# Kernel optimization log

Measured on AMD Instinct MI355X. Metric: run time of the kernel, lower is better.

Reference implementation:

```python
import jax, jax.numpy as jnp
import numpy as np

B, S, D, H, DFF, L = 8192, 9, 3, 3, 2048, 3
HD = D // H  # head dim = 1
EPS = 1e-5


def _ln(x, g, b):
    m = jnp.mean(x, axis=-1, keepdims=True)
    v = jnp.var(x, axis=-1, keepdims=True)
    return (x - m) * jax.lax.rsqrt(v + EPS) * g + b


def _encoder_layer(h, Wqkv, bqkv, Wo, bo, g1, b1, W1, bf1, W2, bf2, g2, b2):
    # h: [B,S,D]; post-norm TransformerEncoderLayer (PyTorch defaults, eval mode)
    qkv = jnp.einsum('bsd,ed->bse', h, Wqkv) + bqkv      # [B,S,3D]
    q, k, v = jnp.split(qkv, 3, axis=-1)
    Bv = h.shape[0]
    q = q.reshape(Bv, S, H, HD) * (1.0 / np.sqrt(HD))
    k = k.reshape(Bv, S, H, HD)
    v = v.reshape(Bv, S, H, HD)
    attn = jax.nn.softmax(jnp.einsum('bqhd,bkhd->bhqk', q, k), axis=-1)
    o = jnp.einsum('bhqk,bkhd->bqhd', attn, v).reshape(Bv, S, D)
    o = jnp.einsum('bsd,od->bso', o, Wo) + bo
    h = _ln(h + o, g1, b1)
    ff = jax.nn.relu(jnp.einsum('bsd,fd->bsf', h, W1) + bf1)  # [B,S,DFF]
    ff = jnp.einsum('bsf,df->bsd', ff, W2) + bf2
    return _ln(h + ff, g2, b2)


def setup_inputs() -> dict:
    key = jax.random.key(0)
    ks = jax.random.split(key, 8)
    sc = 0.3
    return {
        'x': jax.random.normal(ks[0], (B, S * D), dtype=jnp.float32),
        'Wqkv': sc * jax.random.normal(ks[1], (L, 3 * D, D), dtype=jnp.float32),
        'bqkv': jnp.zeros((L, 3 * D), jnp.float32),
        'Wo': sc * jax.random.normal(ks[2], (L, D, D), dtype=jnp.float32),
        'bo': jnp.zeros((L, D), jnp.float32),
        'g1': jnp.ones((L, D), jnp.float32),
        'beta1': jnp.zeros((L, D), jnp.float32),
        'W1': sc * jax.random.normal(ks[3], (L, DFF, D), dtype=jnp.float32),
        'bf1': jnp.zeros((L, DFF), jnp.float32),
        'W2': (sc / np.sqrt(DFF)) * jax.random.normal(ks[4], (L, D, DFF), dtype=jnp.float32),
        'bf2': jnp.zeros((L, D), jnp.float32),
        'g2': jnp.ones((L, D), jnp.float32),
        'beta2': jnp.zeros((L, D), jnp.float32),
        'W': jax.random.normal(ks[5], (D, S), dtype=jnp.float32),
    }


def reference(x, Wqkv, bqkv, Wo, bo, g1, beta1, W1, bf1, W2, bf2, g2, beta2, W):
    h = x.reshape(-1, S, D)                      # split 27-dim state into 9 tokens of 3
    for i in range(L):
        h = _encoder_layer(h, Wqkv[i], bqkv[i], Wo[i], bo[i], g1[i], beta1[i],
                           W1[i], bf1[i], W2[i], bf2[i], g2[i], beta2[i])
    # per-token matmul with W then softmax over the 9 logits (dim=0 of each 9-vector)
    z = jax.nn.softmax(jnp.einsum('bsd,dn->bsn', h, W), axis=-1)  # [B,S,9]
    u = jnp.prod(z, axis=1)                      # elementwise product over 9 tokens
    return jax.nn.softmax(u, axis=-1)            # [B,9] action probabilities
```

## Files before the change

kernel.cpp:

```cpp
#include <hip/hip_runtime.h>
#include <math.h>


constexpr int S   = 9;
constexpr int D   = 3;
constexpr int DFF = 2048;
constexpr int L   = 3;
constexpr int G   = 16;
constexpr int BLK = 256;
constexpr int BPB = BLK / G;
constexpr int FPT = DFF / G;
constexpr float EPS = 1e-5f;

__launch_bounds__(BLK, 2)
__global__ void tf_policy_kernel(const float* __restrict__ x,
                                 const float* __restrict__ Wqkv,
                                 const float* __restrict__ bqkv,
                                 const float* __restrict__ Wo,
                                 const float* __restrict__ bo,
                                 const float* __restrict__ g1,
                                 const float* __restrict__ be1,
                                 const float* __restrict__ W1,
                                 const float* __restrict__ bf1,
                                 const float* __restrict__ W2,
                                 const float* __restrict__ bf2,
                                 const float* __restrict__ g2,
                                 const float* __restrict__ be2,
                                 const float* __restrict__ Wfin,
                                 float* __restrict__ out)
{
    __shared__ float4 s_w1[DFF];
    __shared__ float4 s_w2[DFF];

    const int tid = threadIdx.x;
    const int grp = tid >> 4;
    const int sub = tid & 15;
    const int b   = blockIdx.x * BPB + grp;

    float h[S][D];
    {
        const float* xr = x + (size_t)b * (S * D);
        #pragma unroll
        for (int s = 0; s < S; ++s)
            #pragma unroll
            for (int d = 0; d < D; ++d)
                h[s][d] = xr[s * D + d];
    }

    for (int l = 0; l < L; ++l) {
        __syncthreads();
        {
            const float* w1p = W1  + (size_t)l * DFF * D;
            const float* b1p = bf1 + (size_t)l * DFF;
            const float* w2p = W2  + (size_t)l * D * DFF;
            for (int i = tid; i < DFF; i += BLK) {
                float4 a;
                a.x = w1p[i * 3 + 0];
                a.y = w1p[i * 3 + 1];
                a.z = w1p[i * 3 + 2];
                a.w = b1p[i];
                s_w1[i] = a;
                float4 c;
                c.x = w2p[i];
                c.y = w2p[DFF + i];
                c.z = w2p[2 * DFF + i];
                c.w = 0.f;
                s_w2[i] = c;
            }
        }
        __syncthreads();

        const float* wq = Wqkv + (size_t)l * (3 * D) * D;
        const float* bq = bqkv + (size_t)l * (3 * D);
        float o[S][D];
        #pragma unroll
        for (int hh = 0; hh < 3; ++hh) {
            float q[S], k[S], v[S];
            #pragma unroll
            for (int s = 0; s < S; ++s) {
                q[s] = fmaf(wq[hh * 3 + 0], h[s][0],
                       fmaf(wq[hh * 3 + 1], h[s][1],
                       fmaf(wq[hh * 3 + 2], h[s][2], bq[hh])));
                k[s] = fmaf(wq[(3 + hh) * 3 + 0], h[s][0],
                       fmaf(wq[(3 + hh) * 3 + 1], h[s][1],
                       fmaf(wq[(3 + hh) * 3 + 2], h[s][2], bq[3 + hh])));
                v[s] = fmaf(wq[(6 + hh) * 3 + 0], h[s][0],
                       fmaf(wq[(6 + hh) * 3 + 1], h[s][1],
                       fmaf(wq[(6 + hh) * 3 + 2], h[s][2], bq[6 + hh])));
            }
            #pragma unroll
            for (int qs = 0; qs < S; ++qs) {
                float sc[S];
                float m = -1e30f;
                #pragma unroll
                for (int ks = 0; ks < S; ++ks) {
                    sc[ks] = q[qs] * k[ks];
                    m = fmaxf(m, sc[ks]);
                }
                float sum = 0.f, av = 0.f;
                #pragma unroll
                for (int ks = 0; ks < S; ++ks) {
                    float e = __expf(sc[ks] - m);
                    sum += e;
                    av = fmaf(e, v[ks], av);
                }
                o[qs][hh] = av / sum;
            }
        }

        {
            const float* wo  = Wo  + (size_t)l * D * D;
            const float* bop = bo  + (size_t)l * D;
            const float* gp  = g1  + (size_t)l * D;
            const float* bp  = be1 + (size_t)l * D;
            #pragma unroll
            for (int s = 0; s < S; ++s) {
                float t[D];
                #pragma unroll
                for (int dd = 0; dd < D; ++dd)
                    t[dd] = h[s][dd] + bop[dd] +
                            fmaf(wo[dd * 3 + 0], o[s][0],
                            fmaf(wo[dd * 3 + 1], o[s][1],
                                 wo[dd * 3 + 2] * o[s][2]));
                float m  = (t[0] + t[1] + t[2]) * (1.f / 3.f);
                float d0 = t[0] - m, d1 = t[1] - m, d2 = t[2] - m;
                float va = (d0 * d0 + d1 * d1 + d2 * d2) * (1.f / 3.f);
                float r  = rsqrtf(va + EPS);
                h[s][0] = fmaf(d0 * r, gp[0], bp[0]);
                h[s][1] = fmaf(d1 * r, gp[1], bp[1]);
                h[s][2] = fmaf(d2 * r, gp[2], bp[2]);
            }
        }

        float acc[S][D];
        #pragma unroll
        for (int s = 0; s < S; ++s)
            #pragma unroll
            for (int d = 0; d < D; ++d)
                acc[s][d] = 0.f;

        for (int i = 0; i < FPT; ++i) {
            const int f = i * G + sub;
            const float4 w1 = s_w1[f];
            const float4 w2 = s_w2[f];
            #pragma unroll
            for (int s = 0; s < S; ++s) {
                float t = fmaf(w1.x, h[s][0],
                          fmaf(w1.y, h[s][1],
                          fmaf(w1.z, h[s][2], w1.w)));
                t = fmaxf(t, 0.f);
                acc[s][0] = fmaf(w2.x, t, acc[s][0]);
                acc[s][1] = fmaf(w2.y, t, acc[s][1]);
                acc[s][2] = fmaf(w2.z, t, acc[s][2]);
            }
        }

        #pragma unroll
        for (int mask = 1; mask < G; mask <<= 1) {
            #pragma unroll
            for (int s = 0; s < S; ++s)
                #pragma unroll
                for (int d = 0; d < D; ++d)
                    acc[s][d] += __shfl_xor(acc[s][d], mask, 64);
        }

        {
            const float* b2p = bf2 + (size_t)l * D;
            const float* gp  = g2  + (size_t)l * D;
            const float* bp  = be2 + (size_t)l * D;
            #pragma unroll
            for (int s = 0; s < S; ++s) {
                float t[D];
                #pragma unroll
                for (int dd = 0; dd < D; ++dd)
                    t[dd] = h[s][dd] + acc[s][dd] + b2p[dd];
                float m  = (t[0] + t[1] + t[2]) * (1.f / 3.f);
                float d0 = t[0] - m, d1 = t[1] - m, d2 = t[2] - m;
                float va = (d0 * d0 + d1 * d1 + d2 * d2) * (1.f / 3.f);
                float r  = rsqrtf(va + EPS);
                h[s][0] = fmaf(d0 * r, gp[0], bp[0]);
                h[s][1] = fmaf(d1 * r, gp[1], bp[1]);
                h[s][2] = fmaf(d2 * r, gp[2], bp[2]);
            }
        }
    }

    if (sub == 0) {
        float u[S];
        #pragma unroll
        for (int n = 0; n < S; ++n) u[n] = 1.f;
        #pragma unroll
        for (int s = 0; s < S; ++s) {
            float z[S];
            float m = -1e30f;
            #pragma unroll
            for (int n = 0; n < S; ++n) {
                z[n] = fmaf(h[s][0], Wfin[0 * S + n],
                       fmaf(h[s][1], Wfin[1 * S + n],
                            h[s][2] * Wfin[2 * S + n]));
                m = fmaxf(m, z[n]);
            }
            float sum = 0.f;
            #pragma unroll
            for (int n = 0; n < S; ++n) { z[n] = __expf(z[n] - m); sum += z[n]; }
            float inv = 1.f / sum;
            #pragma unroll
            for (int n = 0; n < S; ++n) u[n] *= z[n] * inv;
        }
        float m = -1e30f;
        #pragma unroll
        for (int n = 0; n < S; ++n) m = fmaxf(m, u[n]);
        float e[S];
        float sum = 0.f;
        #pragma unroll
        for (int n = 0; n < S; ++n) { e[n] = __expf(u[n] - m); sum += e[n]; }
        float inv = 1.f / sum;
        float* op = out + (size_t)b * S;
        #pragma unroll
        for (int n = 0; n < S; ++n) op[n] = e[n] * inv;
    }
}

extern "C" void kernel_launch(void* const* d_in, const int* in_sizes, int n_in,
                              void* d_out, int out_size, void* d_ws, size_t ws_size,
                              hipStream_t stream)
{
    const float* x    = (const float*)d_in[0];
    const float* Wqkv = (const float*)d_in[1];
    const float* bqkv = (const float*)d_in[2];
    const float* Wo   = (const float*)d_in[3];
    const float* bo   = (const float*)d_in[4];
    const float* g1   = (const float*)d_in[5];
    const float* be1  = (const float*)d_in[6];
    const float* W1   = (const float*)d_in[7];
    const float* bf1  = (const float*)d_in[8];
    const float* W2   = (const float*)d_in[9];
    const float* bf2  = (const float*)d_in[10];
    const float* g2   = (const float*)d_in[11];
    const float* be2  = (const float*)d_in[12];
    const float* Wfin = (const float*)d_in[13];
    float* out = (float*)d_out;

    const int B = in_sizes[0] / (S * D);
    const int nblocks = B / BPB;

    tf_policy_kernel<<<nblocks, BLK, 0, stream>>>(
        x, Wqkv, bqkv, Wo, bo, g1, be1, W1, bf1, W2, bf2, g2, be2, Wfin, out);
}
```

Measured before the change: 124.7 us.

## Use packed FP32 FMA for FFN with paired-feature shared memory layout

Restructures the FFN inner loop so each thread processes two hidden features at once using v_pk_fma_f32 inline asm. The shared-memory weight layout changes to paired-feature vectors so each pair's W1, bias and W2 entries load as packed operands. Global loads in the staging loop become 2-wide. The aim is to roughly halve FMA instruction count in the dominant FFN loop. In exchange the kernel carries more vector registers, which may affect occupancy, and the partial sums are added in a different order.

```diff
diff --git a/kernel.cpp b/kernel.cpp
--- a/kernel.cpp
+++ b/kernel.cpp
@@ -10,7 +10,17 @@
 constexpr int BLK = 256;
 constexpr int BPB = BLK / G;
 constexpr int FPT = DFF / G;
+constexpr int PPT = FPT / 2;
 constexpr float EPS = 1e-5f;
+
+typedef float v2f __attribute__((ext_vector_type(2)));
+typedef float v4f __attribute__((ext_vector_type(4)));
+
+__device__ __forceinline__ v2f pk_fma(v2f a, v2f b, v2f c) {
+    v2f d;
+    asm("v_pk_fma_f32 %0, %1, %2, %3" : "=v"(d) : "v"(a), "v"(b), "v"(c));
+    return d;
+}
 
 __launch_bounds__(BLK, 2)
 __global__ void tf_policy_kernel(const float* __restrict__ x,
@@ -29,8 +39,10 @@
                                  const float* __restrict__ Wfin,
                                  float* __restrict__ out)
 {
-    __shared__ float4 s_w1[DFF];
-    __shared__ float4 s_w2[DFF];
+    __shared__ v4f s_a[DFF / 2];
+    __shared__ v4f s_b[DFF / 2];
+    __shared__ v4f s_c[DFF / 2];
+    __shared__ v2f s_d[DFF / 2];
 
     const int tid = threadIdx.x;
     const int grp = tid >> 4;
@@ -53,19 +65,23 @@
             const float* w1p = W1  + (size_t)l * DFF * D;
             const float* b1p = bf1 + (size_t)l * DFF;
             const float* w2p = W2  + (size_t)l * D * DFF;
-            for (int i = tid; i < DFF; i += BLK) {
-                float4 a;
-                a.x = w1p[i * 3 + 0];
-                a.y = w1p[i * 3 + 1];
-                a.z = w1p[i * 3 + 2];
-                a.w = b1p[i];
-                s_w1[i] = a;
-                float4 c;
-                c.x = w2p[i];
-                c.y = w2p[DFF + i];
-                c.z = w2p[2 * DFF + i];
-                c.w = 0.f;
-                s_w2[i] = c;
+            const v2f* w1v = (const v2f*)w1p;
+            const v2f* b1v = (const v2f*)b1p;
+            const v2f* c0v = (const v2f*)w2p;
+            const v2f* c1v = (const v2f*)(w2p + DFF);
+            const v2f* c2v = (const v2f*)(w2p + 2 * DFF);
+            for (int p = tid; p < DFF / 2; p += BLK) {
+                v2f r0 = w1v[3 * p];
+                v2f r1 = w1v[3 * p + 1];
+                v2f r2 = w1v[3 * p + 2];
+                v2f bb = b1v[p];
+                v2f c0 = c0v[p];
+                v2f c1 = c1v[p];
+                v2f c2 = c2v[p];
+                s_a[p] = (v4f){r0.x, r1.y, r0.y, r2.x};
+                s_b[p] = (v4f){r1.x, r2.y, bb.x, bb.y};
+                s_c[p] = (v4f){c0.x, c0.y, c1.x, c1.y};
+                s_d[p] = c2;
             }
         }
         __syncthreads();
@@ -132,28 +148,50 @@
             }
         }
 
+        v2f hb[S][D];
+        #pragma unroll
+        for (int s = 0; s < S; ++s)
+            #pragma unroll
+            for (int d = 0; d < D; ++d)
+                hb[s][d] = (v2f){h[s][d], h[s][d]};
+
+        v2f acc2[S][D];
+        #pragma unroll
+        for (int s = 0; s < S; ++s)
+            #pragma unroll
+            for (int d = 0; d < D; ++d)
+                acc2[s][d] = (v2f){0.f, 0.f};
+
+        #pragma unroll 2
+        for (int i = 0; i < PPT; ++i) {
+            const int p = i * G + sub;
+            const v4f A  = s_a[p];
+            const v4f Bv = s_b[p];
+            const v4f C  = s_c[p];
+            const v2f Dz = s_d[p];
+            const v2f w1x = A.xy,  w1y = A.zw;
+            const v2f w1z = Bv.xy, w1b = Bv.zw;
+            const v2f w2x = C.xy,  w2y = C.zw;
+            #pragma unroll
+            for (int s = 0; s < S; ++s) {
+                v2f t = pk_fma(w1x, hb[s][0],
+                        pk_fma(w1y, hb[s][1],
+                        pk_fma(w1z, hb[s][2], w1b)));
+                t.x = fmaxf(t.x, 0.f);
+                t.y = fmaxf(t.y, 0.f);
+                acc2[s][0] = pk_fma(C.xy, t, acc2[s][0]);
+                acc2[s][1] = pk_fma(w2y, t, acc2[s][1]);
+                acc2[s][2] = pk_fma(Dz, t, acc2[s][2]);
+                (void)w2x;
+            }
+        }
+
         float acc[S][D];
         #pragma unroll
         for (int s = 0; s < S; ++s)
             #pragma unroll
             for (int d = 0; d < D; ++d)
-                acc[s][d] = 0.f;
-
-        for (int i = 0; i < FPT; ++i) {
-            const int f = i * G + sub;
-            const float4 w1 = s_w1[f];
-            const float4 w2 = s_w2[f];
-            #pragma unroll
-            for (int s = 0; s < S; ++s) {
-                float t = fmaf(w1.x, h[s][0],
-                          fmaf(w1.y, h[s][1],
-                          fmaf(w1.z, h[s][2], w1.w)));
-                t = fmaxf(t, 0.f);
-                acc[s][0] = fmaf(w2.x, t, acc[s][0]);
-                acc[s][1] = fmaf(w2.y, t, acc[s][1]);
-                acc[s][2] = fmaf(w2.z, t, acc[s][2]);
-            }
-        }
+                acc[s][d] = acc2[s][d].x + acc2[s][d].y;
 
         #pragma unroll
         for (int mask = 1; mask < G; mask <<= 1) {
```

Result: faster. 119.8 us (-3.9%).
